# Kernel tuning notes

Measured on AMD Instinct MI355X. Metric: run time of the kernel, lower is better.

The kernel has to match this reference:

```python
import jax, jax.numpy as jnp
import numpy as np

K_NEIGHBORS = 3  # init kwarg k_neighbors


def setup_inputs() -> dict:
    key = jax.random.key(0)
    k1, k2 = jax.random.split(key)
    q = jax.random.normal(k1, (75, 640, 21, 21), dtype=jnp.float32)
    S = jax.random.normal(k2, (5, 640, 21, 21), dtype=jnp.float32)
    return {"q": q, "S": S, "qAV_num": 1, "SAV_num": 1, "shot_num": 1}


def reference(q, S, qAV_num, SAV_num, shot_num):
    B, C = q.shape[0], q.shape[1]
    # [B, HW, C], L2-normalize each local descriptor over channels
    qd = q.reshape(B, C, -1).transpose(0, 2, 1)
    qd = qd / jnp.linalg.norm(qd, axis=2, keepdims=True)

    N = S.shape[0]
    sd = S.reshape(N, C, -1).transpose(0, 2, 1)  # [N, HW, C]
    sd = sd / jnp.linalg.norm(sd, axis=2, keepdims=True)
    HW = sd.shape[1]
    M = SAV_num * shot_num * HW
    # group support images into classes: [ncls, C, M]
    sup = sd.reshape(-1, M, C).transpose(0, 2, 1)
    ncls = sup.shape[0]

    # cosine similarity: [B, ncls, HW, M]
    ip = jnp.einsum('bqc,ncm->bnqm', qd, sup)
    # split AV groups: [B//qAV, qAV, ncls, HW, M]
    ip = ip.reshape(B // qAV_num, qAV_num, ncls, HW, M)
    # top-k along the query-descriptor (HW) axis (torch dim=-2)
    topk = jax.lax.top_k(jnp.swapaxes(ip, -1, -2), K_NEIGHBORS)[0]  # [..., M, k]
    img2class = topk.sum(axis=(-1, -2))  # [B', qAV, ncls]
    # geometric mean over the AV axis (dim=1)
    sim = jnp.exp(jnp.mean(jnp.log(img2class), axis=1))  # [B', ncls]
    return sim
```

## Files before the change

### kernel.cpp

```cpp
#include <hip/hip_runtime.h>
#include <hip/hip_bf16.h>


#define B_IMGS 75
#define N_CLS  5
#define C_DIM  640
#define HW     441
#define HWP    448
#define NKT    20
#define NRB    28
#define CHUNK  512
#define TPAD   66

typedef __attribute__((ext_vector_type(8))) short  short8;
typedef __attribute__((ext_vector_type(4))) float  float4v;

__device__ __forceinline__ void ins3(float& t0, float& t1, float& t2, float v) {
    float m  = fminf(t0, v);
    t0 = fmaxf(t0, v);
    float m2 = fminf(t1, m);
    t1 = fmaxf(t1, m);
    t2 = fmaxf(t2, m2);
}

__device__ __forceinline__ void glds16(const __hip_bfloat16* g, __hip_bfloat16* l) {
    __builtin_amdgcn_global_load_lds(
        (const __attribute__((address_space(1))) unsigned int*)g,
        (__attribute__((address_space(3))) unsigned int*)l, 16, 0, 0);
}

__global__ __launch_bounds__(256)
void norm_kernel(const float* __restrict__ q, const float* __restrict__ S,
                 float* __restrict__ invn) {
    __shared__ float part[4][64];
    int bid = blockIdx.x;
    int img = bid / 7;
    int h0  = bid % 7;
    const float* src = (img < B_IMGS)
        ? q + (size_t)img * C_DIM * HW
        : S + (size_t)(img - B_IMGS) * C_DIM * HW;
    int t  = threadIdx.x;
    int hl = t & 63;
    int p  = t >> 6;
    int hw = h0 * 64 + hl;
    int hwc = (hw < HW) ? hw : (HW - 1);

    float ss = 0.f;
    for (int c0 = p * 160; c0 < (p + 1) * 160; c0 += 16) {
        float v[16];
#pragma unroll
        for (int j = 0; j < 16; ++j) v[j] = src[(size_t)(c0 + j) * HW + hwc];
#pragma unroll
        for (int j = 0; j < 16; ++j) ss += v[j] * v[j];
    }
    part[p][hl] = ss;
    __syncthreads();
    if (t < 64) {
        float tot = part[0][t] + part[1][t] + part[2][t] + part[3][t];
        invn[img * HWP + h0 * 64 + t] = (h0 * 64 + t < HW) ? rsqrtf(tot) : 0.f;
    }
}

__global__ __launch_bounds__(256)
void pack_kernel(const float* __restrict__ q, const float* __restrict__ S,
                 const float* __restrict__ invn,
                 __hip_bfloat16* __restrict__ qn2, __hip_bfloat16* __restrict__ sn2) {
    __shared__ __hip_bfloat16 tile[128][TPAD];
    int bid = blockIdx.x;
    int img = bid / 35;
    int rem = bid % 35;
    int h0  = rem / 5;
    int ktg = rem % 5;
    const float* src; __hip_bfloat16* dst;
    if (img < B_IMGS) {
        src = q + (size_t)img * C_DIM * HW;
        dst = qn2 + (size_t)img * NRB * NKT * CHUNK;
    } else {
        src = S + (size_t)(img - B_IMGS) * C_DIM * HW;
        dst = sn2 + (size_t)(img - B_IMGS) * NRB * NKT * CHUNK;
    }
    int t  = threadIdx.x;
    int hl = t & 63;
    int p  = t >> 6;
    int hw = h0 * 64 + hl;
    int hwc = (hw < HW) ? hw : (HW - 1);
    float iv = invn[img * HWP + h0 * 64 + hl];

    for (int c0 = p * 32; c0 < p * 32 + 32; c0 += 8) {
        float v[8];
#pragma unroll
        for (int j = 0; j < 8; ++j)
            v[j] = src[(size_t)(ktg * 128 + c0 + j) * HW + hwc];
#pragma unroll
        for (int j = 0; j < 8; ++j)
            tile[c0 + j][hl] = __float2bfloat16(v[j] * iv);
    }
    __syncthreads();

    int tl  = t & 63;
    int row = tl & 15;
    int oct = tl >> 4;
    int rb  = h0 * 4 + p;
    for (int ktl = 0; ktl < 4; ++ktl) {
        int kt = ktg * 4 + ktl;
        short8 v;
#pragma unroll
        for (int j = 0; j < 8; ++j) {
            __hip_bfloat16 hv = tile[ktl * 32 + oct * 8 + j][p * 16 + row];
            v[j] = *(short*)&hv;
        }
        *(short8*)(dst + ((size_t)rb * NKT + kt) * CHUNK + tl * 8) = v;
    }
}

__global__ __launch_bounds__(256, 2)
void gemm_top3_kernel(const __hip_bfloat16* __restrict__ qn2,
                      const __hip_bfloat16* __restrict__ sn2,
                      float* __restrict__ out) {
    __shared__ __hip_bfloat16 sbuf[2][32 * CHUNK];
    __shared__ float mrg[4][64][3];

    int id  = blockIdx.x;
    int xcd = id & 7;
    int j8  = id >> 3;
    int b   = (j8 / 35) * 8 + xcd;
    if (b >= B_IMGS) return;
    int inner = j8 % 35;
    int n  = inner / 7;
    int mt = inner % 7;

    int tid  = threadIdx.x;
    int w    = tid >> 6;
    int lane = tid & 63;
    int c16  = lane & 15;
    int quad = lane >> 4;
    int frag = lane * 8;

    const __hip_bfloat16* qA = qn2 + (size_t)b * NRB * NKT * CHUNK;
    const __hip_bfloat16* qB = sn2 + ((size_t)n * NRB + mt * 4) * NKT * CHUNK;

    float4v acc[7][4];
#pragma unroll
    for (int r = 0; r < 7; ++r)
#pragma unroll
        for (int j = 0; j < 4; ++j)
            acc[r][j] = (float4v){0.f, 0.f, 0.f, 0.f};

    auto stage = [&](int kt, int pb) {
#pragma unroll
        for (int i = 0; i < 8; ++i) {
            int cid = w * 8 + i;
            const __hip_bfloat16* g = (cid < 28)
                ? qA + ((size_t)cid * NKT + kt) * CHUNK
                : qB + ((size_t)(cid - 28) * NKT + kt) * CHUNK;
            glds16(g + lane * 8, &sbuf[pb][cid * CHUNK + lane * 8]);
        }
    };

    stage(0, 0);
    for (int kt = 0; kt < NKT; ++kt) {
        int p = kt & 1;
        if (kt + 1 < NKT) stage(kt + 1, p ^ 1);
        if (kt + 1 < NKT)
            asm volatile("s_waitcnt vmcnt(8)" ::: "memory");
        else
            asm volatile("s_waitcnt vmcnt(0)" ::: "memory");
        __builtin_amdgcn_s_barrier();

        short8 a[7], bfr[4];
#pragma unroll
        for (int r = 0; r < 7; ++r)
            a[r] = *(const short8*)(&sbuf[p][(r * 4 + w) * CHUNK + frag]);
#pragma unroll
        for (int j = 0; j < 4; ++j)
            bfr[j] = *(const short8*)(&sbuf[p][(28 + j) * CHUNK + frag]);
        asm volatile("s_waitcnt lgkmcnt(0)" ::: "memory");
        __builtin_amdgcn_sched_barrier(0);
        __builtin_amdgcn_s_barrier();

        __builtin_amdgcn_s_setprio(1);
#pragma unroll
        for (int r = 0; r < 7; ++r)
#pragma unroll
            for (int j = 0; j < 4; ++j)
                acc[r][j] = __builtin_amdgcn_mfma_f32_16x16x32_bf16(
                    a[r], bfr[j], acc[r][j], 0, 0, 0);
        __builtin_amdgcn_s_setprio(0);
    }

    float T0[4], T1[4], T2[4];
#pragma unroll
    for (int j = 0; j < 4; ++j) { T0[j] = -1e30f; T1[j] = -1e30f; T2[j] = -1e30f; }
#pragma unroll
    for (int r = 0; r < 7; ++r)
#pragma unroll
        for (int j = 0; j < 4; ++j)
#pragma unroll
            for (int g = 0; g < 4; ++g) {
                int row = r * 64 + w * 16 + quad * 4 + g;
                float v = (row < HW) ? acc[r][j][g] : -1e30f;
                ins3(T0[j], T1[j], T2[j], v);
            }

#pragma unroll
    for (int j = 0; j < 4; ++j) {
#pragma unroll
        for (int d = 16; d <= 32; d <<= 1) {
            float o0 = __shfl_xor(T0[j], d, 64);
            float o1 = __shfl_xor(T1[j], d, 64);
            float o2 = __shfl_xor(T2[j], d, 64);
            ins3(T0[j], T1[j], T2[j], o0);
            ins3(T0[j], T1[j], T2[j], o1);
            ins3(T0[j], T1[j], T2[j], o2);
        }
    }

    if (quad == 0) {
#pragma unroll
        for (int j = 0; j < 4; ++j) {
            mrg[w][j * 16 + c16][0] = T0[j];
            mrg[w][j * 16 + c16][1] = T1[j];
            mrg[w][j * 16 + c16][2] = T2[j];
        }
    }
    __syncthreads();
    if (tid < 64) {
        int col = tid;
        float t0 = mrg[0][col][0], t1 = mrg[0][col][1], t2 = mrg[0][col][2];
#pragma unroll
        for (int ww = 1; ww < 4; ++ww) {
            ins3(t0, t1, t2, mrg[ww][col][0]);
            ins3(t0, t1, t2, mrg[ww][col][1]);
            ins3(t0, t1, t2, mrg[ww][col][2]);
        }
        float s = (mt * 64 + col < HW) ? (t0 + t1 + t2) : 0.f;
#pragma unroll
        for (int d = 32; d >= 1; d >>= 1) s += __shfl_xor(s, d, 64);
        if (tid == 0) atomicAdd(&out[b * N_CLS + n], s);
    }
}

extern "C" void kernel_launch(void* const* d_in, const int* in_sizes, int n_in,
                              void* d_out, int out_size, void* d_ws, size_t ws_size,
                              hipStream_t stream) {
    const float* q = (const float*)d_in[0];
    const float* S = (const float*)d_in[1];
    float* out = (float*)d_out;

    char* ws = (char*)d_ws;
    size_t off = 0;
    __hip_bfloat16* qn2 = (__hip_bfloat16*)(ws + off);
    off += (size_t)B_IMGS * NRB * NKT * CHUNK * 2;  off = (off + 255) & ~(size_t)255;
    __hip_bfloat16* sn2 = (__hip_bfloat16*)(ws + off);
    off += (size_t)N_CLS * NRB * NKT * CHUNK * 2;   off = (off + 255) & ~(size_t)255;
    float* invn = (float*)(ws + off);

    hipMemsetAsync(d_out, 0, (size_t)out_size * sizeof(float), stream);

    norm_kernel<<<dim3(80 * 7), dim3(256), 0, stream>>>(q, S, invn);
    pack_kernel<<<dim3(80 * 7 * 5), dim3(256), 0, stream>>>(q, S, invn, qn2, sn2);
    gemm_top3_kernel<<<dim3(8 * 350), dim3(256), 0, stream>>>(qn2, sn2, out);
}
```

Baseline: 297.7 us.

## Use 8-wave blocks with 4-stage LDS ring and 3-deep prefetch in GEMM

```diff
diff --git a/kernel.cpp b/kernel.cpp
--- a/kernel.cpp
+++ b/kernel.cpp
@@ -11,6 +11,7 @@
 #define NRB    28
 #define CHUNK  512
 #define TPAD   66
+#define SLOT   (32 * CHUNK)
 
 typedef __attribute__((ext_vector_type(8))) short  short8;
 typedef __attribute__((ext_vector_type(4))) float  float4v;
@@ -113,12 +114,13 @@
     }
 }
 
-__global__ __launch_bounds__(256, 2)
+__global__ __launch_bounds__(512, 2)
 void gemm_top3_kernel(const __hip_bfloat16* __restrict__ qn2,
                       const __hip_bfloat16* __restrict__ sn2,
                       float* __restrict__ out) {
-    __shared__ __hip_bfloat16 sbuf[2][32 * CHUNK];
-    __shared__ float mrg[4][64][3];
+    extern __shared__ char smem[];
+    __hip_bfloat16* sbuf = (__hip_bfloat16*)smem;
+    float* mrg = (float*)(smem + (size_t)4 * SLOT * 2);
 
     int id  = blockIdx.x;
     int xcd = id & 7;
@@ -131,6 +133,8 @@
 
     int tid  = threadIdx.x;
     int w    = tid >> 6;
+    int wr   = w & 3;
+    int wc   = w >> 2;
     int lane = tid & 63;
     int c16  = lane & 15;
     int quad = lane >> 4;
@@ -139,41 +143,43 @@
     const __hip_bfloat16* qA = qn2 + (size_t)b * NRB * NKT * CHUNK;
     const __hip_bfloat16* qB = sn2 + ((size_t)n * NRB + mt * 4) * NKT * CHUNK;
 
-    float4v acc[7][4];
+    float4v acc[7][2];
 #pragma unroll
     for (int r = 0; r < 7; ++r)
 #pragma unroll
-        for (int j = 0; j < 4; ++j)
+        for (int j = 0; j < 2; ++j)
             acc[r][j] = (float4v){0.f, 0.f, 0.f, 0.f};
 
     auto stage = [&](int kt, int pb) {
 #pragma unroll
-        for (int i = 0; i < 8; ++i) {
-            int cid = w * 8 + i;
+        for (int i = 0; i < 4; ++i) {
+            int cid = w * 4 + i;
             const __hip_bfloat16* g = (cid < 28)
                 ? qA + ((size_t)cid * NKT + kt) * CHUNK
                 : qB + ((size_t)(cid - 28) * NKT + kt) * CHUNK;
-            glds16(g + lane * 8, &sbuf[pb][cid * CHUNK + lane * 8]);
+            glds16(g + lane * 8, sbuf + (size_t)pb * SLOT + cid * CHUNK + lane * 8);
         }
     };
 
     stage(0, 0);
+    stage(1, 1);
+    stage(2, 2);
     for (int kt = 0; kt < NKT; ++kt) {
-        int p = kt & 1;
-        if (kt + 1 < NKT) stage(kt + 1, p ^ 1);
-        if (kt + 1 < NKT)
-            asm volatile("s_waitcnt vmcnt(8)" ::: "memory");
-        else
-            asm volatile("s_waitcnt vmcnt(0)" ::: "memory");
+        if (kt + 3 < NKT) stage(kt + 3, (kt + 3) & 3);
+        if (kt < NKT - 3)      asm volatile("s_waitcnt vmcnt(12)" ::: "memory");
+        else if (kt == NKT - 3) asm volatile("s_waitcnt vmcnt(8)" ::: "memory");
+        else if (kt == NKT - 2) asm volatile("s_waitcnt vmcnt(4)" ::: "memory");
+        else                    asm volatile("s_waitcnt vmcnt(0)" ::: "memory");
         __builtin_amdgcn_s_barrier();
 
-        short8 a[7], bfr[4];
+        const __hip_bfloat16* sb = sbuf + (size_t)(kt & 3) * SLOT;
+        short8 a[7], bb[2];
 #pragma unroll
         for (int r = 0; r < 7; ++r)
-            a[r] = *(const short8*)(&sbuf[p][(r * 4 + w) * CHUNK + frag]);
-#pragma unroll
-        for (int j = 0; j < 4; ++j)
-            bfr[j] = *(const short8*)(&sbuf[p][(28 + j) * CHUNK + frag]);
+            a[r] = *(const short8*)(sb + (r * 4 + wr) * CHUNK + frag);
+#pragma unroll
+        for (int j = 0; j < 2; ++j)
+            bb[j] = *(const short8*)(sb + (28 + wc * 2 + j) * CHUNK + frag);
         asm volatile("s_waitcnt lgkmcnt(0)" ::: "memory");
         __builtin_amdgcn_sched_barrier(0);
         __builtin_amdgcn_s_barrier();
@@ -182,28 +188,28 @@
 #pragma unroll
         for (int r = 0; r < 7; ++r)
 #pragma unroll
-            for (int j = 0; j < 4; ++j)
+            for (int j = 0; j < 2; ++j)
                 acc[r][j] = __builtin_amdgcn_mfma_f32_16x16x32_bf16(
-                    a[r], bfr[j], acc[r][j], 0, 0, 0);
+                    a[r], bb[j], acc[r][j], 0, 0, 0);
         __builtin_amdgcn_s_setprio(0);
     }
 
-    float T0[4], T1[4], T2[4];
-#pragma unroll
-    for (int j = 0; j < 4; ++j) { T0[j] = -1e30f; T1[j] = -1e30f; T2[j] = -1e30f; }
+    float T0[2], T1[2], T2[2];
+#pragma unroll
+    for (int j = 0; j < 2; ++j) { T0[j] = -1e30f; T1[j] = -1e30f; T2[j] = -1e30f; }
 #pragma unroll
     for (int r = 0; r < 7; ++r)
 #pragma unroll
-        for (int j = 0; j < 4; ++j)
+        for (int j = 0; j < 2; ++j)
 #pragma unroll
             for (int g = 0; g < 4; ++g) {
-                int row = r * 64 + w * 16 + quad * 4 + g;
+                int row = r * 64 + wr * 16 + quad * 4 + g;
                 float v = (row < HW) ? acc[r][j][g] : -1e30f;
                 ins3(T0[j], T1[j], T2[j], v);
             }
 
 #pragma unroll
-    for (int j = 0; j < 4; ++j) {
+    for (int j = 0; j < 2; ++j) {
 #pragma unroll
         for (int d = 16; d <= 32; d <<= 1) {
             float o0 = __shfl_xor(T0[j], d, 64);
@@ -217,21 +223,24 @@
 
     if (quad == 0) {
 #pragma unroll
-        for (int j = 0; j < 4; ++j) {
-            mrg[w][j * 16 + c16][0] = T0[j];
-            mrg[w][j * 16 + c16][1] = T1[j];
-            mrg[w][j * 16 + c16][2] = T2[j];
+        for (int j = 0; j < 2; ++j) {
+            float* m = mrg + ((size_t)w * 32 + j * 16 + c16) * 3;
+            m[0] = T0[j]; m[1] = T1[j]; m[2] = T2[j];
         }
     }
     __syncthreads();
     if (tid < 64) {
-        int col = tid;
-        float t0 = mrg[0][col][0], t1 = mrg[0][col][1], t2 = mrg[0][col][2];
-#pragma unroll
-        for (int ww = 1; ww < 4; ++ww) {
-            ins3(t0, t1, t2, mrg[ww][col][0]);
-            ins3(t0, t1, t2, mrg[ww][col][1]);
-            ins3(t0, t1, t2, mrg[ww][col][2]);
+        int col  = tid;
+        int wcg  = col >> 5;
+        int rest = col & 31;
+        const float* m0 = mrg + ((size_t)(wcg * 4 + 0) * 32 + rest) * 3;
+        float t0 = m0[0], t1 = m0[1], t2 = m0[2];
+#pragma unroll
+        for (int wrr = 1; wrr < 4; ++wrr) {
+            const float* m = mrg + ((size_t)(wcg * 4 + wrr) * 32 + rest) * 3;
+            ins3(t0, t1, t2, m[0]);
+            ins3(t0, t1, t2, m[1]);
+            ins3(t0, t1, t2, m[2]);
         }
         float s = (mt * 64 + col < HW) ? (t0 + t1 + t2) : 0.f;
 #pragma unroll
@@ -255,9 +264,18 @@
     off += (size_t)N_CLS * NRB * NKT * CHUNK * 2;   off = (off + 255) & ~(size_t)255;
     float* invn = (float*)(ws + off);
 
+    const size_t gemm_lds = (size_t)4 * SLOT * 2 + 8 * 32 * 3 * sizeof(float);
+    static bool attr_set = false;
+    if (!attr_set) {
+        (void)hipFuncSetAttribute((const void*)gemm_top3_kernel,
+                                  hipFuncAttributeMaxDynamicSharedMemorySize,
+                                  (int)gemm_lds);
+        attr_set = true;
+    }
+
     hipMemsetAsync(d_out, 0, (size_t)out_size * sizeof(float), stream);
 
     norm_kernel<<<dim3(80 * 7), dim3(256), 0, stream>>>(q, S, invn);
     pack_kernel<<<dim3(80 * 7 * 5), dim3(256), 0, stream>>>(q, S, invn, qn2, sn2);
-    gemm_top3_kernel<<<dim3(8 * 350), dim3(256), 0, stream>>>(qn2, sn2, out);
-}
+    gemm_top3_kernel<<<dim3(8 * 350), dim3(512), gemm_lds, stream>>>(qn2, sn2, out);
+}
```

New measurement: 310.6 us. 1.04x slower.
